# Optimization experiments

Hardware: AMD Instinct MI355X
Metric: run time of the kernel (lower is better)

Reference implementation:

```python
import jax, jax.numpy as jnp
import numpy as np

B, N, K, D = 8, 4096, 16, 256


def layer_norm(x, g, b, eps=1e-5):
    m = jnp.mean(x, axis=-1, keepdims=True)
    v = jnp.var(x, axis=-1, keepdims=True)
    return (x - m) * jax.lax.rsqrt(v + eps) * g + b


def setup_inputs() -> dict:
    key = jax.random.key(0)
    ks = jax.random.split(key, 8)

    def lin(k, fi, fo):
        return (jax.random.normal(k, (fi, fo), jnp.float32) / np.sqrt(fi).astype(np.float32),
                jnp.zeros((fo,), jnp.float32))

    coordinates = jax.random.normal(ks[0], (B, N, 3), jnp.float32)
    W1, b1 = lin(ks[1], 10, D // 4)
    W2, b2 = lin(ks[2], D // 4, D // 2)
    W3, b3 = lin(ks[3], D // 2, D)
    Wa1, ba1 = lin(ks[4], D, D)
    Wa2, ba2 = lin(ks[5], D, D)
    return {
        'coordinates': coordinates,
        'W1': W1, 'b1': b1, 'g1': jnp.ones((D // 4,)), 'be1': jnp.zeros((D // 4,)),
        'W2': W2, 'b2': b2, 'g2': jnp.ones((D // 2,)), 'be2': jnp.zeros((D // 2,)),
        'W3': W3, 'b3': b3, 'g3': jnp.ones((D,)), 'be3': jnp.zeros((D,)),
        'Wa1': Wa1, 'ba1': ba1, 'ga1': jnp.ones((D,)), 'bea1': jnp.zeros((D,)),
        'Wa2': Wa2, 'ba2': ba2,
    }


def reference(coordinates, W1, b1, g1, be1, W2, b2, g2, be2, W3, b3, g3, be3,
              Wa1, ba1, ga1, bea1, Wa2, ba2):
    # kNN via squared-distance matrix (monotone in Euclidean distance)
    sq = jnp.sum(coordinates * coordinates, axis=-1)  # [B,N]
    d2 = sq[:, :, None] + sq[:, None, :] - 2.0 * jnp.einsum('bnd,bmd->bnm', coordinates, coordinates)
    _, idx = jax.lax.top_k(-d2, K)  # smallest K distances, [B,N,K]

    nbr = jax.vmap(lambda c, i: c[i])(coordinates, idx)  # [B,N,K,3]
    rel = nbr - coordinates[:, :, None, :]               # relative positions
    dist = jnp.linalg.norm(rel, axis=-1, keepdims=True)  # [B,N,K,1]
    rn = rel / (dist + 1e-6)
    axy = jnp.arctan2(rn[..., 1], rn[..., 0])[..., None]
    axz = jnp.arctan2(rn[..., 2], rn[..., 0])[..., None]
    ayz = jnp.arctan2(rn[..., 2], rn[..., 1])[..., None]
    geom = jnp.concatenate([dist, rel, axy, axz, ayz, rn], axis=-1)  # [B,N,K,10]

    # encoder MLP
    h = jax.nn.relu(layer_norm(geom @ W1 + b1, g1, be1))
    h = jax.nn.relu(layer_norm(h @ W2 + b2, g2, be2))
    h = layer_norm(h @ W3 + b3, g3, be3)

    agg = jnp.mean(h, axis=2)  # mean over neighbors -> [B,N,D]

    # aggregator MLP
    out = jax.nn.relu(layer_norm(agg @ Wa1 + ba1, ga1, bea1)) @ Wa2 + ba2
    return out
```

## Files before the change

kernel.cpp:

```cpp
#include <hip/hip_runtime.h>
#include <hip/hip_bf16.h>
#include <math.h>

#define BB 8
#define NN 4096
#define KK 16
#define DD 256

typedef __hip_bfloat16 bf16;
typedef _Float16 half8 __attribute__((ext_vector_type(8)));
typedef float f32x4 __attribute__((ext_vector_type(4)));

union HFU { _Float16 h; unsigned short u; };
__device__ __forceinline__ unsigned short f2h(float x) { HFU v; v.h = (_Float16)x; return v.u; }

#define CONV_TOTAL 273344
#define O_COORD 0
#define O_W1 98304
#define O_b1 98944
#define O_g1 99008
#define O_be1 99072
#define O_W2 99136
#define O_b2 107328
#define O_g2 107456
#define O_be2 107584
#define O_W3 107712
#define O_b3 140480
#define O_g3 140736
#define O_be3 140992
#define O_Wa1 141248
#define O_ba1 206784
#define O_ga1 207040
#define O_bea1 207296
#define O_Wa2 207552
#define O_ba2 273088

#define F_W1 0
#define F_W2 2048
#define F_W3 10240
#define F_A1 43008
#define F_A2 108544
#define FRAG_TOTAL 174080

struct SrcPtrs {
  const void* p[19];
};

__global__ __launch_bounds__(256) void convert_kernel(SrcPtrs sp, float* __restrict__ dst) {
  static constexpr int OFF[20] = {
      0,      98304,  98944,  99008,  99072,  99136,  107328, 107456, 107584,
      107712, 140480, 140736, 140992, 141248, 206784, 207040, 207296, 207552,
      273088, 273344};
  const int i = blockIdx.x * 256 + threadIdx.x;
  if (i >= CONV_TOTAL) return;
  const unsigned tag = ((const unsigned*)sp.p[3])[0];
  const bool isb = (tag == 0x3F803F80u);
  int s = 0;
#pragma unroll
  for (int j = 1; j < 19; j++)
    if (i >= OFF[j]) s = j;
  const int local = i - OFF[s];
  float v = isb ? __bfloat162float(((const bf16*)sp.p[s])[local])
                : ((const float*)sp.p[s])[local];
  dst[i] = v;
}

__global__ __launch_bounds__(256) void swizzle_kernel(const float* __restrict__ conv,
                                                      unsigned short* __restrict__ frag) {
  const int t = blockIdx.x * 256 + threadIdx.x;
  if (t >= FRAG_TOTAL) return;
  int l, e;
  if (t < 2048) { l = 0; e = t; }
  else if (t < 10240) { l = 1; e = t - 2048; }
  else if (t < 43008) { l = 2; e = t - 10240; }
  else if (t < 108544) { l = 3; e = t - 43008; }
  else { l = 4; e = t - 108544; }
  static constexpr int WOFF[5] = {O_W1, O_W2, O_W3, O_Wa1, O_Wa2};
  static constexpr int NDIM[5] = {64, 128, 256, 256, 256};
  static constexpr int NTC[5] = {4, 8, 16, 16, 16};
  static constexpr int KREAL[5] = {10, 64, 128, 256, 256};
  static constexpr int HOFF[5] = {F_W1, F_W2, F_W3, F_A1, F_A2};
  const int j = e & 7;
  const int lane = (e >> 3) & 63;
  const int tile = e >> 9;
  const int nt = tile % NTC[l];
  const int kt = tile / NTC[l];
  const int k = kt * 32 + (lane >> 4) * 8 + j;
  const int n = nt * 16 + (lane & 15);
  float w = (k < KREAL[l]) ? conv[WOFF[l] + k * NDIM[l] + n] : 0.0f;
  frag[HOFF[l] + e] = f2h(w);
}

__device__ __forceinline__ float sq3_rn(float x, float y, float z) {
  return __fadd_rn(__fadd_rn(__fmul_rn(x, x), __fmul_rn(y, y)), __fmul_rn(z, z));
}
__device__ __forceinline__ float dot3_rn(float ax, float ay, float az, float bx, float by, float bz) {
  return __fadd_rn(__fadd_rn(__fmul_rn(ax, bx), __fmul_rn(ay, by)), __fmul_rn(az, bz));
}
__device__ __forceinline__ unsigned f2ord(float f) {
  unsigned u = __float_as_uint(f);
  return (u & 0x80000000u) ? ~u : (u | 0x80000000u);
}
__device__ __forceinline__ float ord2f(unsigned o) {
  unsigned u = (o & 0x80000000u) ? (o & 0x7FFFFFFFu) : ~o;
  return __uint_as_float(u);
}

__device__ __forceinline__ float bcast_f(float v, int srclane) {
  return __uint_as_float((unsigned)__builtin_amdgcn_readlane(__float_as_int(v), srclane));
}
__device__ __forceinline__ unsigned long long dpp_shr1_u64(unsigned long long x) {
  int lo = __builtin_amdgcn_update_dpp(0, (int)(unsigned)x, 0x111, 0xf, 0xf, false);
  int hi = __builtin_amdgcn_update_dpp(0, (int)(unsigned)(x >> 32), 0x111, 0xf, 0xf, false);
  return ((unsigned long long)(unsigned)hi << 32) | (unsigned)lo;
}

__global__ __launch_bounds__(256) void prep_kernel(const float* __restrict__ conv,
                                                   float4* __restrict__ soa) {
  const int i = blockIdx.x * 256 + threadIdx.x;
  if (i >= BB * NN) return;
  const float* c = conv + O_COORD + (size_t)i * 3;
  float x = c[0], y = c[1], z = c[2];
  soa[i] = make_float4(x, y, z, sq3_rn(x, y, z));
}

__global__ __launch_bounds__(256) void knn_wave_kernel(const float4* __restrict__ soa,
                                                       int* __restrict__ idx_out) {
  const int lane = threadIdx.x & 63;
  const int wid = (blockIdx.x * 256 + threadIdx.x) >> 6;
  const int q0 = wid * 4;
  const int b = q0 >> 12;
  const float4* P = soa + (size_t)b * NN;

  float cx[4], cy[4], cz[4], sqn[4];
#pragma unroll
  for (int j = 0; j < 4; j++) {
    float4 c = P[(q0 + j) & (NN - 1)];
    cx[j] = c.x; cy[j] = c.y; cz[j] = c.z; sqn[j] = c.w;
  }

  unsigned long long R[4];
  float tauf[4];

  float4 c0 = P[lane];
  float4 cnext = P[64 + lane];

#pragma unroll
  for (int j = 0; j < 4; j++) {
    float dot = dot3_rn(cx[j], cy[j], cz[j], c0.x, c0.y, c0.z);
    float d2 = __fsub_rn(__fadd_rn(sqn[j], c0.w), __fmul_rn(2.0f, dot));
    unsigned long long key = (((unsigned long long)f2ord(d2)) << 32) | (unsigned)lane;
#pragma unroll
    for (int k = 2; k <= 64; k <<= 1) {
#pragma unroll
      for (int jj = k >> 1; jj > 0; jj >>= 1) {
        unsigned long long v = __shfl_xor(key, jj, 64);
        bool asc = ((lane & k) == 0);
        bool up = ((lane & jj) != 0);
        unsigned long long mn = (key < v) ? key : v;
        unsigned long long mx2 = (key < v) ? v : key;
        key = (up == asc) ? mx2 : mn;
      }
    }
    R[j] = key;
    tauf[j] = ord2f((unsigned)((unsigned long long)__builtin_amdgcn_readlane(
                        (int)(unsigned)(R[j] >> 32), 15)));
  }

  for (int bt = 1; bt < 64; bt++) {
    const float4 c = cnext;
    if (bt < 63) cnext = P[(bt + 1) * 64 + lane];
    const int m0 = bt * 64;
    float d2v[4];
    unsigned long long pm[4];
#pragma unroll
    for (int j = 0; j < 4; j++) {
      float dot = dot3_rn(cx[j], cy[j], cz[j], c.x, c.y, c.z);
      d2v[j] = __fsub_rn(__fadd_rn(sqn[j], c.w), __fmul_rn(2.0f, dot));
      pm[j] = __ballot(d2v[j] <= tauf[j]);
    }
    if (pm[0] | pm[1] | pm[2] | pm[3]) {
#pragma unroll
      for (int j = 0; j < 4; j++) {
        unsigned long long pmask = pm[j];
        if (pmask) {
          do {
            int s = __builtin_ctzll(pmask);
            pmask &= pmask - 1;
            float d2s = bcast_f(d2v[j], s);
            unsigned long long nk =
                (((unsigned long long)f2ord(d2s)) << 32) | (unsigned)(m0 + s);
            unsigned long long lt = __ballot(R[j] < nk) & 0xFFFFull;
            int pos = __builtin_popcountll(lt);
            unsigned long long prev = dpp_shr1_u64(R[j]);
            if (lane == pos) R[j] = nk;
            else if (lane > pos) R[j] = prev;
          } while (pmask);
          tauf[j] = ord2f((unsigned)((unsigned long long)__builtin_amdgcn_readlane(
                              (int)(unsigned)(R[j] >> 32), 15)));
        }
      }
    }
  }

#pragma unroll
  for (int j = 0; j < 4; j++)
    if (lane < KK)
      idx_out[(size_t)(q0 + j) * KK + lane] = (int)(R[j] & 0xFFFFFFFFull);
}

template <int KT>
__device__ __forceinline__ void load_afrags(half8* A, const unsigned short* lF,
                                            int rowe, int lane) {
#pragma unroll
  for (int kt = 0; kt < KT; kt++) {
    int off = (lane & 15) * rowe + kt * 32 + (lane >> 4) * 8;
    A[kt] = *reinterpret_cast<const half8*>(lF + off);
  }
}

template <int NT>
__device__ __forceinline__ void init_acc(f32x4* acc, const float* __restrict__ bias,
                                         int lane) {
  const int col = lane & 15;
#pragma unroll
  for (int nt = 0; nt < NT; nt++) {
    float bv = bias[nt * 16 + col];
    acc[nt] = {bv, bv, bv, bv};
  }
}

template <int KT, int NT>
__device__ __forceinline__ void gemm_acc(f32x4* acc, const half8* A,
                                         const unsigned short* bb, int lane) {
#pragma unroll
  for (int kt = 0; kt < KT; kt++)
#pragma unroll
    for (int nt = 0; nt < NT; nt++) {
      const half8 bf = *reinterpret_cast<const half8*>(bb + (kt * NT + nt) * 512 + lane * 8);
      acc[nt] = __builtin_amdgcn_mfma_f32_16x16x32_f16(A[kt], bf, acc[nt], 0, 0, 0);
    }
}

template <int NT>
__device__ __forceinline__ void ln_stats(const f32x4* acc, float* m, float* rs) {
  float s[4] = {0.f, 0.f, 0.f, 0.f}, s2[4] = {0.f, 0.f, 0.f, 0.f};
#pragma unroll
  for (int nt = 0; nt < NT; nt++)
#pragma unroll
    for (int r = 0; r < 4; r++) {
      float v = acc[nt][r];
      s[r] += v;
      s2[r] += v * v;
    }
#pragma unroll
  for (int msk = 1; msk <= 8; msk <<= 1)
#pragma unroll
    for (int r = 0; r < 4; r++) {
      s[r] += __shfl_xor(s[r], msk, 64);
      s2[r] += __shfl_xor(s2[r], msk, 64);
    }
  const float invN = 1.0f / (NT * 16);
#pragma unroll
  for (int r = 0; r < 4; r++) {
    m[r] = s[r] * invN;
    float var = s2[r] * invN - m[r] * m[r];
    rs[r] = rsqrtf(var + 1e-5f);
  }
}

template <int NT, bool RELU>
__device__ __forceinline__ void ln_store(const f32x4* acc, const float* m, const float* rs,
                                         const float* __restrict__ g, const float* __restrict__ be,
                                         unsigned short* lF, int rowe, int lane) {
  const int col = lane & 15;
  const int rbase = (lane >> 4) * 4;
#pragma unroll
  for (int nt = 0; nt < NT; nt++) {
    float gv = g[nt * 16 + col], bv = be[nt * 16 + col];
#pragma unroll
    for (int r = 0; r < 4; r++) {
      float v = (acc[nt][r] - m[r]) * rs[r] * gv + bv;
      if (RELU) v = fmaxf(v, 0.0f);
      lF[(rbase + r) * rowe + nt * 16 + col] = f2h(v);
    }
  }
}

__device__ __forceinline__ void stage_b(unsigned short* bbuf,
                                        const unsigned short* __restrict__ src,
                                        int n_u4, int tid) {
  const uint4* s = reinterpret_cast<const uint4*>(src);
  uint4* d = reinterpret_cast<uint4*>(bbuf);
  for (int i = tid; i < n_u4; i += 256) d[i] = s[i];
}

#define ROWE_E 136
#define PSTR_E (16 * ROWE_E)

__global__ __launch_bounds__(256, 3) void encoder_mfma(
    const float* __restrict__ conv, const int* __restrict__ nbr,
    const unsigned short* __restrict__ frag, unsigned short* __restrict__ agF) {
  __shared__ unsigned short planes[4 * PSTR_E];
  __shared__ unsigned short Bbuf[16384];
  const int tid = threadIdx.x;
  const int lane = tid & 63;
  const int wave = tid >> 6;
  const int point = blockIdx.x * 4 + wave;
  const int b = point >> 12;
  const int n = point & (NN - 1);
  const float* cb = conv + O_COORD + (size_t)b * NN * 3;
  unsigned short* lF = planes + wave * PSTR_E;

  {
    int pl = tid >> 6, row = (tid >> 2) & 15, part = tid & 3;
    *reinterpret_cast<uint4*>(planes + pl * PSTR_E + row * ROWE_E + part * 8) =
        make_uint4(0u, 0u, 0u, 0u);
    stage_b(Bbuf, frag + F_W1, 1280, tid);
  }
  __syncthreads();

  if (lane < 16) {
    float cx = cb[n * 3 + 0], cy = cb[n * 3 + 1], cz = cb[n * 3 + 2];
    int id = nbr[(size_t)point * KK + lane];
    float rx = __fsub_rn(cb[id * 3 + 0], cx);
    float ry = __fsub_rn(cb[id * 3 + 1], cy);
    float rz = __fsub_rn(cb[id * 3 + 2], cz);
    float dist = __fsqrt_rn(sq3_rn(rx, ry, rz));
    float den = __fadd_rn(dist, 1e-6f);
    float ux = __fdiv_rn(rx, den), uy = __fdiv_rn(ry, den), uz = __fdiv_rn(rz, den);
    float ge[10];
    ge[0] = dist; ge[1] = rx; ge[2] = ry; ge[3] = rz;
    ge[4] = atan2f(uy, ux); ge[5] = atan2f(uz, ux); ge[6] = atan2f(uz, uy);
    ge[7] = ux; ge[8] = uy; ge[9] = uz;
#pragma unroll
    for (int c = 0; c < 10; c++) lF[lane * ROWE_E + c] = f2h(ge[c]);
  }

  float m[4], rs[4];
  {
    half8 A[1];
    load_afrags<1>(A, lF, ROWE_E, lane);
    f32x4 acc1[4];
    init_acc<4>(acc1, conv + O_b1, lane);
    gemm_acc<1, 4>(acc1, A, Bbuf, lane);
    ln_stats<4>(acc1, m, rs);
    ln_store<4, true>(acc1, m, rs, conv + O_g1, conv + O_be1, lF, ROWE_E, lane);
  }
  {
    half8 A[2];
    load_afrags<2>(A, lF, ROWE_E, lane);
    f32x4 acc2[8];
    init_acc<8>(acc2, conv + O_b2, lane);
    gemm_acc<2, 8>(acc2, A, Bbuf + 2048, lane);
    ln_stats<8>(acc2, m, rs);
    ln_store<8, true>(acc2, m, rs, conv + O_g2, conv + O_be2, lF, ROWE_E, lane);
  }
  half8 A3[4];
  load_afrags<4>(A3, lF, ROWE_E, lane);
  f32x4 acc[16];
  init_acc<16>(acc, conv + O_b3, lane);
  __syncthreads();
  stage_b(Bbuf, frag + F_W3, 2048, tid);
  __syncthreads();
  gemm_acc<2, 16>(acc, A3, Bbuf, lane);
  __syncthreads();
  stage_b(Bbuf, frag + F_W3 + 16384, 2048, tid);
  __syncthreads();
  gemm_acc<2, 16>(acc, A3 + 2, Bbuf, lane);

  {
    ln_stats<16>(acc, m, rs);
    const int col = lane & 15;
    float sv[16];
#pragma unroll
    for (int nt = 0; nt < 16; nt++) {
      float gv = conv[O_g3 + nt * 16 + col], bv = conv[O_be3 + nt * 16 + col];
      float s = 0.f;
#pragma unroll
      for (int r = 0; r < 4; r++) s += (acc[nt][r] - m[r]) * rs[r] * gv + bv;
      s += __shfl_xor(s, 16, 64);
      s += __shfl_xor(s, 32, 64);
      sv[nt] = s * (1.0f / 16.0f);
    }
    if (lane < 16) {
      size_t base = (size_t)point * DD;
#pragma unroll
      for (int nt = 0; nt < 16; nt++) agF[base + nt * 16 + lane] = f2h(sv[nt]);
    }
  }
}

#define ROWE_A 264

__global__ __launch_bounds__(256) void aggmlp_mfma(
    const float* __restrict__ conv, const unsigned short* __restrict__ agF,
    const unsigned short* __restrict__ a1, const unsigned short* __restrict__ a2,
    const unsigned* __restrict__ g1raw, void* __restrict__ out) {
  __shared__ unsigned short lds[4][16 * ROWE_A];
  const int lane = threadIdx.x & 63;
  const int wave = threadIdx.x >> 6;
  const int row0 = (blockIdx.x * 4 + wave) * 16;
  unsigned short* lF = lds[wave];

#pragma unroll
  for (int t = 0; t < 8; t++) {
    int v = t * 64 + lane;
    int row = v >> 5;
    int c0 = (v & 31) * 8;
    *reinterpret_cast<uint4*>(lF + row * ROWE_A + c0) =
        *reinterpret_cast<const uint4*>(agF + ((size_t)(row0 + row) * DD + c0));
  }
  __syncthreads();

  float m[4], rs[4];
  f32x4 acc[16];
  {
    half8 A[8];
    load_afrags<8>(A, lF, ROWE_A, lane);
    init_acc<16>(acc, conv + O_ba1, lane);
    gemm_acc<8, 16>(acc, A, a1, lane);
    ln_stats<16>(acc, m, rs);
    ln_store<16, true>(acc, m, rs, conv + O_ga1, conv + O_bea1, lF, ROWE_A, lane);
  }
  __syncthreads();
  {
    half8 A[8];
    load_afrags<8>(A, lF, ROWE_A, lane);
    init_acc<16>(acc, conv + O_ba2, lane);
    gemm_acc<8, 16>(acc, A, a2, lane);
  }
  const bool isb = (g1raw[0] == 0x3F803F80u);
  const int col = lane & 15;
  const int rbase = (lane >> 4) * 4;
  if (isb) {
    bf16* o = (bf16*)out;
#pragma unroll
    for (int nt = 0; nt < 16; nt++)
#pragma unroll
      for (int r = 0; r < 4; r++)
        o[(size_t)(row0 + rbase + r) * DD + nt * 16 + col] = __float2bfloat16(acc[nt][r]);
  } else {
    float* o = (float*)out;
#pragma unroll
    for (int nt = 0; nt < 16; nt++)
#pragma unroll
      for (int r = 0; r < 4; r++)
        o[(size_t)(row0 + rbase + r) * DD + nt * 16 + col] = acc[nt][r];
  }
}

extern "C" void kernel_launch(void* const* d_in, const int* in_sizes, int n_in,
                              void* d_out, int out_size, void* d_ws, size_t ws_size,
                              hipStream_t stream) {
  char* ws = (char*)d_ws;
  float* conv = (float*)ws;
  int* idx_ws = (int*)(ws + 1093376);
  unsigned short* agF = (unsigned short*)(ws + 3190528);
  unsigned short* frag = (unsigned short*)(ws + 19967744);
  float4* soa = (float4*)(ws + 20315904);

  SrcPtrs sp;
  for (int i = 0; i < 19; i++) sp.p[i] = d_in[i];

  convert_kernel<<<(CONV_TOTAL + 255) / 256, 256, 0, stream>>>(sp, conv);
  swizzle_kernel<<<(FRAG_TOTAL + 255) / 256, 256, 0, stream>>>(conv, frag);
  prep_kernel<<<(BB * NN + 255) / 256, 256, 0, stream>>>(conv, soa);

  knn_wave_kernel<<<BB * NN / 16, 256, 0, stream>>>(soa, idx_ws);

  encoder_mfma<<<BB * NN / 4, 256, 0, stream>>>(conv, idx_ws, frag, agF);

  aggmlp_mfma<<<BB * NN / 64, 256, 0, stream>>>(conv, agF, frag + F_A1, frag + F_A2,
                                                (const unsigned*)d_in[3], d_out);
}
```

Before: 419.6 us.

## Batch kNN candidate insertion into pending buffer merged via bitonic sort

Replaces per-candidate serial insertion into the 16-entry top-K list with compaction of passing candidates into a per-query pending buffer held in lanes 16..63, using mbcnt and ds_permute/bpermute. When the buffer would overflow, or at the end, it runs a full 64-lane bitonic sort that merges the pending entries with the current top-16 and refreshes the threshold. This cuts the serialized per-candidate loop but lets the threshold go stale between merges, so more candidates pass the filter, and each merge costs a full 64-wide sort.

```diff
diff --git a/kernel.cpp b/kernel.cpp
--- a/kernel.cpp
+++ b/kernel.cpp
@@ -106,13 +106,20 @@
   return __uint_as_float(u);
 }
 
-__device__ __forceinline__ float bcast_f(float v, int srclane) {
-  return __uint_as_float((unsigned)__builtin_amdgcn_readlane(__float_as_int(v), srclane));
-}
-__device__ __forceinline__ unsigned long long dpp_shr1_u64(unsigned long long x) {
-  int lo = __builtin_amdgcn_update_dpp(0, (int)(unsigned)x, 0x111, 0xf, 0xf, false);
-  int hi = __builtin_amdgcn_update_dpp(0, (int)(unsigned)(x >> 32), 0x111, 0xf, 0xf, false);
-  return ((unsigned long long)(unsigned)hi << 32) | (unsigned)lo;
+__device__ __forceinline__ unsigned long long bitonic64(unsigned long long key, int lane) {
+#pragma unroll
+  for (int k = 2; k <= 64; k <<= 1) {
+#pragma unroll
+    for (int jj = k >> 1; jj > 0; jj >>= 1) {
+      unsigned long long v = __shfl_xor(key, jj, 64);
+      bool asc = ((lane & k) == 0);
+      bool up = ((lane & jj) != 0);
+      unsigned long long mn = (key < v) ? key : v;
+      unsigned long long mx2 = (key < v) ? v : key;
+      key = (up == asc) ? mx2 : mn;
+    }
+  }
+  return key;
 }
 
 __global__ __launch_bounds__(256) void prep_kernel(const float* __restrict__ conv,
@@ -139,32 +146,47 @@
     cx[j] = c.x; cy[j] = c.y; cz[j] = c.z; sqn[j] = c.w;
   }
 
-  unsigned long long R[4];
+  unsigned long long R[4], pend[4];
   float tauf[4];
+  int A[4] = {0, 0, 0, 0};
+#pragma unroll
+  for (int j = 0; j < 4; j++) pend[j] = ~0ull;
 
   float4 c0 = P[lane];
   float4 cnext = P[64 + lane];
+
+  auto MERGE = [&](int j) {
+    unsigned long long key =
+        (lane < 16) ? R[j] : ((lane < 16 + A[j]) ? pend[j] : ~0ull);
+    key = bitonic64(key, lane);
+    R[j] = key;
+    tauf[j] = ord2f((unsigned)(unsigned long long)__builtin_amdgcn_readlane(
+        (int)(unsigned)(key >> 32), 15));
+    A[j] = 0;
+  };
+
+  auto APPEND = [&](int j, unsigned long long msk, int cc, unsigned long long key) {
+    unsigned rank = __builtin_amdgcn_mbcnt_hi(
+        (unsigned)(msk >> 32), __builtin_amdgcn_mbcnt_lo((unsigned)msk, 0u));
+    const bool flag = ((msk >> lane) & 1ull) != 0;
+    const int dst = flag ? (16 + A[j] + (int)rank) : (lane & 15);
+    int src = __builtin_amdgcn_ds_permute(dst << 2, lane) & 63;
+    unsigned lo = (unsigned)__builtin_amdgcn_ds_bpermute(src << 2, (int)(unsigned)key);
+    unsigned hi = (unsigned)__builtin_amdgcn_ds_bpermute(src << 2, (int)(unsigned)(key >> 32));
+    const bool cons = (lane >= 16 + A[j]) && (lane < 16 + A[j] + cc);
+    if (cons) pend[j] = (((unsigned long long)hi) << 32) | lo;
+    A[j] += cc;
+  };
 
 #pragma unroll
   for (int j = 0; j < 4; j++) {
     float dot = dot3_rn(cx[j], cy[j], cz[j], c0.x, c0.y, c0.z);
     float d2 = __fsub_rn(__fadd_rn(sqn[j], c0.w), __fmul_rn(2.0f, dot));
     unsigned long long key = (((unsigned long long)f2ord(d2)) << 32) | (unsigned)lane;
-#pragma unroll
-    for (int k = 2; k <= 64; k <<= 1) {
-#pragma unroll
-      for (int jj = k >> 1; jj > 0; jj >>= 1) {
-        unsigned long long v = __shfl_xor(key, jj, 64);
-        bool asc = ((lane & k) == 0);
-        bool up = ((lane & jj) != 0);
-        unsigned long long mn = (key < v) ? key : v;
-        unsigned long long mx2 = (key < v) ? v : key;
-        key = (up == asc) ? mx2 : mn;
-      }
-    }
+    key = bitonic64(key, lane);
     R[j] = key;
-    tauf[j] = ord2f((unsigned)((unsigned long long)__builtin_amdgcn_readlane(
-                        (int)(unsigned)(R[j] >> 32), 15)));
+    tauf[j] = ord2f((unsigned)(unsigned long long)__builtin_amdgcn_readlane(
+        (int)(unsigned)(key >> 32), 15));
   }
 
   for (int bt = 1; bt < 64; bt++) {
@@ -179,34 +201,34 @@
       d2v[j] = __fsub_rn(__fadd_rn(sqn[j], c.w), __fmul_rn(2.0f, dot));
       pm[j] = __ballot(d2v[j] <= tauf[j]);
     }
-    if (pm[0] | pm[1] | pm[2] | pm[3]) {
-#pragma unroll
-      for (int j = 0; j < 4; j++) {
-        unsigned long long pmask = pm[j];
-        if (pmask) {
-          do {
-            int s = __builtin_ctzll(pmask);
-            pmask &= pmask - 1;
-            float d2s = bcast_f(d2v[j], s);
-            unsigned long long nk =
-                (((unsigned long long)f2ord(d2s)) << 32) | (unsigned)(m0 + s);
-            unsigned long long lt = __ballot(R[j] < nk) & 0xFFFFull;
-            int pos = __builtin_popcountll(lt);
-            unsigned long long prev = dpp_shr1_u64(R[j]);
-            if (lane == pos) R[j] = nk;
-            else if (lane > pos) R[j] = prev;
-          } while (pmask);
-          tauf[j] = ord2f((unsigned)((unsigned long long)__builtin_amdgcn_readlane(
-                              (int)(unsigned)(R[j] >> 32), 15)));
+    if (!(pm[0] | pm[1] | pm[2] | pm[3])) continue;
+#pragma unroll
+    for (int j = 0; j < 4; j++) {
+      unsigned long long rem = pm[j];
+      if (!rem) continue;
+      const unsigned long long key =
+          (((unsigned long long)f2ord(d2v[j])) << 32) | (unsigned)(m0 + lane);
+      int cc = __builtin_popcountll(rem);
+      while (A[j] + cc > 48) {
+        if (A[j] == 0) {
+          unsigned long long take = rem & 0xFFFFFFFFull;
+          APPEND(j, take, __builtin_popcountll(take), key);
+          rem ^= take;
         }
+        MERGE(j);
+        rem &= __ballot(d2v[j] <= tauf[j]);
+        cc = __builtin_popcountll(rem);
       }
-    }
-  }
-
-#pragma unroll
-  for (int j = 0; j < 4; j++)
+      APPEND(j, rem, cc, key);
+    }
+  }
+
+#pragma unroll
+  for (int j = 0; j < 4; j++) {
+    if (A[j]) MERGE(j);
     if (lane < KK)
       idx_out[(size_t)(q0 + j) * KK + lane] = (int)(R[j] & 0xFFFFFFFFull);
+  }
 }
 
 template <int KT>
```

Measured after the change: 419.6 us. No clear change (+0.0%).

## Sort points by Morton cell so kNN scans spatially near tiles first

Applied to the files above, without the earlier changes.

Adds a per-batch kernel that bins points into an 8x8x8 grid, orders the bins by Morton code with a shared-memory histogram and scan, and writes the points in sorted order along with their original indices. The kNN kernel then processes queries in this sorted order and starts its tile scan at the query's own tile before wrapping around. Close candidates are found early, which tightens the threshold sooner and cuts down on the serial insertion work. In exchange there is an extra single-block-per-batch sort kernel and a recomputation of squared norms inside the inner loop.

```diff
diff --git a/kernel.cpp b/kernel.cpp
--- a/kernel.cpp
+++ b/kernel.cpp
@@ -115,13 +115,64 @@
   return ((unsigned long long)(unsigned)hi << 32) | (unsigned)lo;
 }
 
-__global__ __launch_bounds__(256) void prep_kernel(const float* __restrict__ conv,
-                                                   float4* __restrict__ soa) {
-  const int i = blockIdx.x * 256 + threadIdx.x;
-  if (i >= BB * NN) return;
-  const float* c = conv + O_COORD + (size_t)i * 3;
-  float x = c[0], y = c[1], z = c[2];
-  soa[i] = make_float4(x, y, z, sq3_rn(x, y, z));
+__device__ __forceinline__ unsigned long long bitonic64(unsigned long long key, int lane) {
+#pragma unroll
+  for (int k = 2; k <= 64; k <<= 1) {
+#pragma unroll
+    for (int jj = k >> 1; jj > 0; jj >>= 1) {
+      unsigned long long v = __shfl_xor(key, jj, 64);
+      bool asc = ((lane & k) == 0);
+      bool up = ((lane & jj) != 0);
+      unsigned long long mn = (key < v) ? key : v;
+      unsigned long long mx2 = (key < v) ? v : key;
+      key = (up == asc) ? mx2 : mn;
+    }
+  }
+  return key;
+}
+
+__global__ __launch_bounds__(512) void cellsort_kernel(const float* __restrict__ conv,
+                                                       float4* __restrict__ sorted) {
+  __shared__ unsigned hist[512];
+  __shared__ unsigned scanb[512];
+  const int b = blockIdx.x;
+  const int tid = threadIdx.x;
+  const float* cb = conv + O_COORD + (size_t)b * NN * 3;
+  hist[tid] = 0;
+  __syncthreads();
+  float xs[8], ys[8], zs[8];
+  int cell[8];
+  unsigned rank[8];
+#pragma unroll
+  for (int u = 0; u < 8; u++) {
+    int p = u * 512 + tid;
+    float x = cb[p * 3 + 0], y = cb[p * 3 + 1], z = cb[p * 3 + 2];
+    xs[u] = x; ys[u] = y; zs[u] = z;
+    int ix = min(7, max(0, (int)floorf(x + 4.0f)));
+    int iy = min(7, max(0, (int)floorf(y + 4.0f)));
+    int iz = min(7, max(0, (int)floorf(z + 4.0f)));
+    int m = ((ix & 1) | ((ix & 2) << 2) | ((ix & 4) << 4)) |
+            (((iy & 1) | ((iy & 2) << 2) | ((iy & 4) << 4)) << 1) |
+            (((iz & 1) | ((iz & 2) << 2) | ((iz & 4) << 4)) << 2);
+    cell[u] = m;
+    rank[u] = atomicAdd(&hist[m], 1u);
+  }
+  __syncthreads();
+  scanb[tid] = hist[tid];
+  __syncthreads();
+  for (int off = 1; off < 512; off <<= 1) {
+    unsigned t = (tid >= off) ? scanb[tid - off] : 0u;
+    __syncthreads();
+    scanb[tid] += t;
+    __syncthreads();
+  }
+#pragma unroll
+  for (int u = 0; u < 8; u++) {
+    unsigned base = scanb[cell[u]] - hist[cell[u]];
+    unsigned pos = base + rank[u];
+    sorted[(size_t)b * NN + pos] =
+        make_float4(xs[u], ys[u], zs[u], __int_as_float(u * 512 + tid));
+  }
 }
 
 __global__ __launch_bounds__(256) void knn_wave_kernel(const float4* __restrict__ soa,
@@ -131,52 +182,51 @@
   const int q0 = wid * 4;
   const int b = q0 >> 12;
   const float4* P = soa + (size_t)b * NN;
+  const int qr = q0 & (NN - 1);
+  const int base = qr >> 6;
 
   float cx[4], cy[4], cz[4], sqn[4];
+  int qix[4];
 #pragma unroll
   for (int j = 0; j < 4; j++) {
-    float4 c = P[(q0 + j) & (NN - 1)];
-    cx[j] = c.x; cy[j] = c.y; cz[j] = c.z; sqn[j] = c.w;
+    float4 c = P[qr + j];
+    cx[j] = c.x; cy[j] = c.y; cz[j] = c.z;
+    sqn[j] = sq3_rn(c.x, c.y, c.z);
+    qix[j] = __float_as_int(c.w);
   }
 
   unsigned long long R[4];
   float tauf[4];
 
-  float4 c0 = P[lane];
-  float4 cnext = P[64 + lane];
-
-#pragma unroll
-  for (int j = 0; j < 4; j++) {
-    float dot = dot3_rn(cx[j], cy[j], cz[j], c0.x, c0.y, c0.z);
-    float d2 = __fsub_rn(__fadd_rn(sqn[j], c0.w), __fmul_rn(2.0f, dot));
-    unsigned long long key = (((unsigned long long)f2ord(d2)) << 32) | (unsigned)lane;
-#pragma unroll
-    for (int k = 2; k <= 64; k <<= 1) {
-#pragma unroll
-      for (int jj = k >> 1; jj > 0; jj >>= 1) {
-        unsigned long long v = __shfl_xor(key, jj, 64);
-        bool asc = ((lane & k) == 0);
-        bool up = ((lane & jj) != 0);
-        unsigned long long mn = (key < v) ? key : v;
-        unsigned long long mx2 = (key < v) ? v : key;
-        key = (up == asc) ? mx2 : mn;
-      }
-    }
-    R[j] = key;
-    tauf[j] = ord2f((unsigned)((unsigned long long)__builtin_amdgcn_readlane(
-                        (int)(unsigned)(R[j] >> 32), 15)));
-  }
-
-  for (int bt = 1; bt < 64; bt++) {
+  float4 c0 = P[base * 64 + lane];
+  float4 cnext = P[((base + 1) & 63) * 64 + lane];
+
+  {
+    const float cw0 = sq3_rn(c0.x, c0.y, c0.z);
+    const unsigned mi0 = (unsigned)__float_as_int(c0.w);
+#pragma unroll
+    for (int j = 0; j < 4; j++) {
+      float dot = dot3_rn(cx[j], cy[j], cz[j], c0.x, c0.y, c0.z);
+      float d2 = __fsub_rn(__fadd_rn(sqn[j], cw0), __fmul_rn(2.0f, dot));
+      unsigned long long key = (((unsigned long long)f2ord(d2)) << 32) | mi0;
+      key = bitonic64(key, lane);
+      R[j] = key;
+      tauf[j] = ord2f((unsigned)(unsigned long long)__builtin_amdgcn_readlane(
+          (int)(unsigned)(key >> 32), 15));
+    }
+  }
+
+  for (int t = 1; t < 64; t++) {
     const float4 c = cnext;
-    if (bt < 63) cnext = P[(bt + 1) * 64 + lane];
-    const int m0 = bt * 64;
+    if (t < 63) cnext = P[((base + t + 1) & 63) * 64 + lane];
+    const float cw = sq3_rn(c.x, c.y, c.z);
+    const int midx = __float_as_int(c.w);
     float d2v[4];
     unsigned long long pm[4];
 #pragma unroll
     for (int j = 0; j < 4; j++) {
       float dot = dot3_rn(cx[j], cy[j], cz[j], c.x, c.y, c.z);
-      d2v[j] = __fsub_rn(__fadd_rn(sqn[j], c.w), __fmul_rn(2.0f, dot));
+      d2v[j] = __fsub_rn(__fadd_rn(sqn[j], c.w * 0.0f + cw), __fmul_rn(2.0f, dot));
       pm[j] = __ballot(d2v[j] <= tauf[j]);
     }
     if (pm[0] | pm[1] | pm[2] | pm[3]) {
@@ -188,16 +238,17 @@
             int s = __builtin_ctzll(pmask);
             pmask &= pmask - 1;
             float d2s = bcast_f(d2v[j], s);
+            int mi = __builtin_amdgcn_readlane(midx, s);
             unsigned long long nk =
-                (((unsigned long long)f2ord(d2s)) << 32) | (unsigned)(m0 + s);
+                (((unsigned long long)f2ord(d2s)) << 32) | (unsigned)mi;
             unsigned long long lt = __ballot(R[j] < nk) & 0xFFFFull;
             int pos = __builtin_popcountll(lt);
             unsigned long long prev = dpp_shr1_u64(R[j]);
             if (lane == pos) R[j] = nk;
             else if (lane > pos) R[j] = prev;
           } while (pmask);
-          tauf[j] = ord2f((unsigned)((unsigned long long)__builtin_amdgcn_readlane(
-                              (int)(unsigned)(R[j] >> 32), 15)));
+          tauf[j] = ord2f((unsigned)(unsigned long long)__builtin_amdgcn_readlane(
+              (int)(unsigned)(R[j] >> 32), 15));
         }
       }
     }
@@ -206,7 +257,8 @@
 #pragma unroll
   for (int j = 0; j < 4; j++)
     if (lane < KK)
-      idx_out[(size_t)(q0 + j) * KK + lane] = (int)(R[j] & 0xFFFFFFFFull);
+      idx_out[((size_t)b * NN + (unsigned)qix[j]) * KK + lane] =
+          (int)(R[j] & 0xFFFFFFFFull);
 }
 
 template <int KT>
@@ -458,16 +510,16 @@
   int* idx_ws = (int*)(ws + 1093376);
   unsigned short* agF = (unsigned short*)(ws + 3190528);
   unsigned short* frag = (unsigned short*)(ws + 19967744);
-  float4* soa = (float4*)(ws + 20315904);
+  float4* sorted = (float4*)(ws + 20315904);
 
   SrcPtrs sp;
   for (int i = 0; i < 19; i++) sp.p[i] = d_in[i];
 
   convert_kernel<<<(CONV_TOTAL + 255) / 256, 256, 0, stream>>>(sp, conv);
   swizzle_kernel<<<(FRAG_TOTAL + 255) / 256, 256, 0, stream>>>(conv, frag);
-  prep_kernel<<<(BB * NN + 255) / 256, 256, 0, stream>>>(conv, soa);
-
-  knn_wave_kernel<<<BB * NN / 16, 256, 0, stream>>>(soa, idx_ws);
+  cellsort_kernel<<<BB, 512, 0, stream>>>(conv, sorted);
+
+  knn_wave_kernel<<<BB * NN / 16, 256, 0, stream>>>(sorted, idx_ws);
 
   encoder_mfma<<<BB * NN / 4, 256, 0, stream>>>(conv, idx_ws, frag, agF);
 
```

Measured after the change: 456.0 us. +8.7%, slower.
